# Kernel optimization log

Measured on AMD Instinct MI355X. Metric: run time of the kernel, lower is better.

## Reference

```python
import jax, jax.numpy as jnp
import numpy as np
from math import sqrt

N_HEADS = 16

def _rope(t, freqs):
    # t: [b, n, l, hd]; freqs: [l, hd//2, 2] (real, imag of unit rotations)
    b, n, l, hd = t.shape
    t2 = t.reshape(b, n, l, hd // 2, 2)
    tr, ti = t2[..., 0], t2[..., 1]
    fr, fi = freqs[..., 0], freqs[..., 1]  # broadcast over b, n
    out_r = tr * fr - ti * fi
    out_i = tr * fi + ti * fr
    return jnp.stack([out_r, out_i], axis=-1).reshape(b, n, l, hd)

def setup_inputs() -> dict:
    key = jax.random.key(0)
    ks = jax.random.split(key, 6)
    B, L, D = 2, 2048, 1024
    HD = D // N_HEADS
    x = jax.random.normal(ks[0], (B, L, D), dtype=jnp.float32)
    # proper rotary frequencies: theta_i = 10000^{-2i/hd}, angle = pos * theta
    inv = 1.0 / (10000.0 ** (np.arange(0, HD, 2, dtype=np.float32) / HD))  # [HD//2]
    ang = np.arange(L, dtype=np.float32)[:, None] * inv[None, :]           # [L, HD//2]
    freqs = jnp.asarray(np.stack([np.cos(ang), np.sin(ang)], axis=-1))     # [L, HD//2, 2]
    # additive causal mask
    causal = jnp.tril(jnp.ones((L, L), dtype=bool))
    attention_mask = jnp.where(causal, 0.0, -1e9).astype(jnp.float32)[None, None]
    init = 1.0 / sqrt(D)
    Wq = jax.random.normal(ks[1], (D, D), dtype=jnp.float32) * init
    Wk = jax.random.normal(ks[2], (D, D), dtype=jnp.float32) * init
    Wv = jax.random.normal(ks[3], (D, D), dtype=jnp.float32) * init
    Wo = jax.random.normal(ks[4], (D, D), dtype=jnp.float32) * init
    return {"x": x, "freqs": freqs, "attention_mask": attention_mask,
            "Wq": Wq, "Wk": Wk, "Wv": Wv, "Wo": Wo}

def reference(x, freqs, attention_mask, Wq, Wk, Wv, Wo):
    b, l, d = x.shape
    n = N_HEADS
    hd = d // n
    scale = sqrt(hd)

    def split_heads(t):  # [b, l, d] -> [b, n, l, hd]
        return t.reshape(b, l, n, hd).transpose(0, 2, 1, 3)

    q = split_heads(x @ Wq.T)
    k = split_heads(x @ Wk.T)
    v = split_heads(x @ Wv.T)
    q = _rope(q, freqs)
    k = _rope(k, freqs)
    scores = jnp.einsum('bnqd,bnkd->bnqk', q, k) / scale
    attn = jax.nn.softmax(scores + attention_mask, axis=-1)
    out = jnp.einsum('bnqk,bnkd->bnqd', attn, v)
    out = out.transpose(0, 2, 1, 3).reshape(b, l, d)
    return out @ Wo.T
```

## Files before the change

kernel.cpp:

```cpp
#include <hip/hip_runtime.h>
#include <stdint.h>

#define LSEQ 2048
#define DMODEL 1024
#define NHEADS 16
#define HDIM 64
#define MROWS 4096

typedef __attribute__((ext_vector_type(8))) short short8;
typedef __attribute__((ext_vector_type(4))) float f32x4;
typedef __attribute__((ext_vector_type(16))) float f32x16;

static __device__ __forceinline__ unsigned short f2bf(float f) {
    unsigned u = __builtin_bit_cast(unsigned, f);
    u += 0x7fffu + ((u >> 16) & 1u);
    return (unsigned short)(u >> 16);
}
static __device__ __forceinline__ unsigned packbf2(float a, float b) {
    return (unsigned)f2bf(a) | ((unsigned)f2bf(b) << 16);
}

static __device__ __forceinline__ void gl2lds16(const unsigned short* g, unsigned short* l) {
    __builtin_amdgcn_global_load_lds(
        (const __attribute__((address_space(1))) unsigned int*)g,
        (__attribute__((address_space(3))) unsigned int*)l, 16, 0, 0);
}

__global__ void cast_all(const float* __restrict__ x,  const float* __restrict__ Wq,
                         const float* __restrict__ Wk, const float* __restrict__ Wv,
                         const float* __restrict__ Wo,
                         unsigned short* __restrict__ xb,
                         unsigned short* __restrict__ wqkv,
                         unsigned short* __restrict__ wo) {
    int i = blockIdx.x * blockDim.x + threadIdx.x;
    const float4* src;
    ushort4* dst;
    if (i < 1048576) {
        src = (const float4*)x + i;
        dst = (ushort4*)xb + i;
    } else {
        int t = i - 1048576;
        int w = t >> 18;
        int j = t & 262143;
        const float* s = (w == 0) ? Wq : (w == 1) ? Wk : (w == 2) ? Wv : Wo;
        src = (const float4*)s + j;
        dst = (w == 3) ? ((ushort4*)wo + j) : ((ushort4*)wqkv + (size_t)w * 262144 + j);
    }
    float4 v = *src;
    ushort4 o;
    o.x = f2bf(v.x); o.y = f2bf(v.y); o.z = f2bf(v.z); o.w = f2bf(v.w);
    *dst = o;
}

template <int TM, bool OUT_BF16>
__global__ __launch_bounds__(256) void gemm_nt(const unsigned short* __restrict__ A,
                                               const unsigned short* __restrict__ Bw,
                                               void* __restrict__ C,
                                               int Kdim, int ldc) {
    constexpr int WM = TM / 2;
    __shared__ unsigned short As[TM * 32];
    __shared__ unsigned short Bs[128 * 32];
    int tid = threadIdx.x;
    int lane = tid & 63, wave = tid >> 6;
    int row16 = lane & 15, quad = lane >> 4;
    int wm = wave & 1, wn = wave >> 1;
    int m0 = blockIdx.x * TM;
    int n0 = blockIdx.y * 128;

    int srow = wave * 16 + (lane >> 2);
    int scol = (lane & 3) * 8;
    const unsigned short* Ag = A  + (size_t)(m0 + srow) * Kdim + scol;
    const unsigned short* Bg = Bw + (size_t)(n0 + srow) * Kdim + scol;
    unsigned short* Asw = As + wave * 512;
    unsigned short* Bsw = Bs + wave * 512;

    f32x4 acc[WM / 16][4];
    #pragma unroll
    for (int i = 0; i < WM / 16; ++i)
        #pragma unroll
        for (int j = 0; j < 4; ++j) acc[i][j] = (f32x4){0.f, 0.f, 0.f, 0.f};

    for (int k0 = 0; k0 < Kdim; k0 += 32) {
        #pragma unroll
        for (int i = 0; i < TM / 64; ++i)
            gl2lds16(Ag + (size_t)i * 64 * Kdim + k0, Asw + i * 2048);
        gl2lds16(Bg + k0, Bsw);
        gl2lds16(Bg + (size_t)64 * Kdim + k0, Bsw + 2048);
        __syncthreads();

        short8 af[WM / 16], bf_[4];
        #pragma unroll
        for (int mi = 0; mi < WM / 16; ++mi)
            af[mi] = *(const short8*)(As + (wm * WM + mi * 16 + row16) * 32 + quad * 8);
        #pragma unroll
        for (int ni = 0; ni < 4; ++ni)
            bf_[ni] = *(const short8*)(Bs + (wn * 64 + ni * 16 + row16) * 32 + quad * 8);
        #pragma unroll
        for (int mi = 0; mi < WM / 16; ++mi)
            #pragma unroll
            for (int ni = 0; ni < 4; ++ni)
                acc[mi][ni] = __builtin_amdgcn_mfma_f32_16x16x32_bf16(af[mi], bf_[ni], acc[mi][ni], 0, 0, 0);
        __syncthreads();
    }

    int orow = m0 + wm * WM + quad * 4;
    int ocol = n0 + wn * 64 + row16;
    #pragma unroll
    for (int mi = 0; mi < WM / 16; ++mi)
        #pragma unroll
        for (int ni = 0; ni < 4; ++ni)
            #pragma unroll
            for (int r = 0; r < 4; ++r) {
                size_t idx = (size_t)(orow + mi * 16 + r) * ldc + (ocol + ni * 16);
                if (OUT_BF16) ((unsigned short*)C)[idx] = f2bf(acc[mi][ni][r]);
                else          ((float*)C)[idx]          = acc[mi][ni][r];
            }
}

#define QKV_PHASE(VN, T, DO_STAGE)                                          \
  {                                                                         \
    asm volatile("s_waitcnt vmcnt(" #VN ")" ::: "memory");                  \
    __builtin_amdgcn_s_barrier();                                           \
    __builtin_amdgcn_sched_barrier(0);                                      \
    if (DO_STAGE) {                                                         \
      int t3 = (T) + 3;                                                     \
      int ws = (t3 & 3) * 16384;                                            \
      const unsigned short* asrc = AgL + t3 * 32;                           \
      const unsigned short* bsrc = BgL + t3 * 32;                           \
      gl2lds16(asrc,                        lds + ws + stA);                \
      gl2lds16(asrc + (size_t)128 * DMODEL, lds + ws + stA + 4096);         \
      gl2lds16(bsrc,                        lds + ws + stB);                \
      gl2lds16(bsrc + (size_t)128 * DMODEL, lds + ws + stB + 4096);         \
    }                                                                       \
    {                                                                       \
      int rs = ((T) & 3) * 16384;                                           \
      const unsigned short* Ar = lds + rs + rdA;                            \
      const unsigned short* Br = lds + rs + 8192 + rdB;                     \
      short8 bfr[4];                                                        \
      _Pragma("unroll")                                                     \
      for (int j = 0; j < 4; ++j) bfr[j] = *(const short8*)(Br + j * 512);  \
      _Pragma("unroll")                                                     \
      for (int q = 0; q < 2; ++q) {                                         \
        short8 af[4];                                                       \
        _Pragma("unroll")                                                   \
        for (int i = 0; i < 4; ++i)                                         \
          af[i] = *(const short8*)(Ar + q * 2048 + i * 512);                \
        __builtin_amdgcn_s_setprio(1);                                      \
        _Pragma("unroll")                                                   \
        for (int i = 0; i < 4; ++i)                                         \
          _Pragma("unroll")                                                 \
          for (int j = 0; j < 4; ++j)                                       \
            acc[q * 4 + i][j] = __builtin_amdgcn_mfma_f32_16x16x32_bf16(    \
                af[i], bfr[j], acc[q * 4 + i][j], 0, 0, 0);                 \
        __builtin_amdgcn_s_setprio(0);                                      \
      }                                                                     \
    }                                                                       \
  }

__global__ __launch_bounds__(512, 2) void gemm_qkv(const unsigned short* __restrict__ A,
                                                   const unsigned short* __restrict__ Bw,
                                                   const float* __restrict__ freqs,
                                                   unsigned short* __restrict__ qh,
                                                   unsigned short* __restrict__ kh,
                                                   unsigned short* __restrict__ vt) {
    extern __shared__ unsigned short lds[];

    int tid  = threadIdx.x;
    int lane = tid & 63, wave = tid >> 6;
    int row16 = lane & 15, quad = lane >> 4;
    int wm = wave & 1, wn = wave >> 1;

    int id  = blockIdx.x;
    int gid = (id & 7) * 24 + (id >> 3);
    int bx = gid / 12, by = gid % 12;
    int m0 = bx * 256, n0 = by * 256;

    int off0 = tid * 16;
    int g = off0 ^ (((off0 >> 7) & 3) << 4);
    int srow = g >> 6;
    int scol = (g & 63) >> 1;
    const unsigned short* AgL = A  + (size_t)(m0 + srow) * DMODEL + scol;
    const unsigned short* BgL = Bw + (size_t)(n0 + srow) * DMODEL + scol;

    int stA = wave * 512;
    int stB = 8192 + wave * 512;

    int sw  = ((row16 >> 1) & 3) << 4;
    int rdA = ((((wm * 128 + row16) * 64) + quad * 16) ^ sw) >> 1;
    int rdB = ((((wn *  64 + row16) * 64) + quad * 16) ^ sw) >> 1;

    f32x4 acc[8][4];
    #pragma unroll
    for (int i = 0; i < 8; ++i)
        #pragma unroll
        for (int j = 0; j < 4; ++j) acc[i][j] = (f32x4){0.f, 0.f, 0.f, 0.f};

    #pragma unroll
    for (int p = 0; p < 3; ++p) {
        int ws = p * 16384;
        const unsigned short* asrc = AgL + p * 32;
        const unsigned short* bsrc = BgL + p * 32;
        gl2lds16(asrc,                        lds + ws + stA);
        gl2lds16(asrc + (size_t)128 * DMODEL, lds + ws + stA + 4096);
        gl2lds16(bsrc,                        lds + ws + stB);
        gl2lds16(bsrc + (size_t)128 * DMODEL, lds + ws + stB + 4096);
    }

    for (int t = 0; t < 30; ++t) {
        QKV_PHASE(8, t, (t < 29))
    }
    QKV_PHASE(4, 30, false)
    QKV_PHASE(0, 31, false)

    int region = n0 >> 10;
    int b = m0 >> 11;
    int orow0 = m0 + wm * 128 + quad * 4;
    int ocol0 = n0 + wn * 64 + row16;

    if (region < 2) {
        unsigned short* dst = region ? kh : qh;
        float sgn = (row16 & 1) ? 1.f : -1.f;
        #pragma unroll
        for (int nf = 0; nf < 4; ++nf) {
            int c = ocol0 - region * 1024 + nf * 16;
            int head = c >> 6, d = c & 63, ii = d >> 1;
            unsigned short* hb = dst + ((size_t)(b * NHEADS + head) * LSEQ) * HDIM + d;
            #pragma unroll
            for (int mf = 0; mf < 8; ++mf)
                #pragma unroll
                for (int r = 0; r < 4; ++r) {
                    int l = (orow0 + mf * 16 + r) & 2047;
                    float own = acc[mf][nf][r];
                    float par = __shfl_xor(own, 1);
                    float2 f = *(const float2*)(freqs + ((size_t)l * 32 + ii) * 2);
                    float out = own * f.x + par * (sgn * f.y);
                    hb[(size_t)l * HDIM] = f2bf(out);
                }
        }
    } else {
        #pragma unroll
        for (int nf = 0; nf < 4; ++nf) {
            int c = ocol0 - 2048 + nf * 16;
            int head = c >> 6, d = c & 63;
            size_t vbase = ((size_t)(b * NHEADS + head) * HDIM + d) * LSEQ;
            #pragma unroll
            for (int mf = 0; mf < 8; ++mf) {
                int l0 = (orow0 + mf * 16) & 2047;
                ushort4 o;
                o.x = f2bf(acc[mf][nf][0]);
                o.y = f2bf(acc[mf][nf][1]);
                o.z = f2bf(acc[mf][nf][2]);
                o.w = f2bf(acc[mf][nf][3]);
                *(ushort4*)(vt + vbase + l0) = o;
            }
        }
    }
}

__global__ __launch_bounds__(256, 4) void attn_flash(const unsigned short* __restrict__ qh,
                                                     const unsigned short* __restrict__ kh,
                                                     const unsigned short* __restrict__ vt,
                                                     unsigned short* __restrict__ oh) {
    __shared__ char smem[16896];
    unsigned short* Kbuf = (unsigned short*)smem;
    unsigned short* Vbuf = (unsigned short*)(smem + 8192);
    float* mO = (float*)smem;
    float* mL = (float*)(smem + 16384);
    const float CS = 0.18033688011112042f;
    const float CB = 28.853900817779268f;

    int lane = threadIdx.x & 63;
    int wave = threadIdx.x >> 6;
    int l31 = lane & 31;
    int h   = lane >> 5;
    int kq  = wave >> 1, qq = wave & 1;

    int id  = blockIdx.x;
    int xcd = id & 7;
    int bn  = xcd * 4 + ((id >> 3) & 3);
    int s   = id >> 5;
    int u = s & 7, rnd = s >> 3;
    int qb = (rnd == 0) ? (31 - u) : (rnd == 1) ? (16 + u) : (rnd == 2) ? (15 - u) : u;
    int b = bn >> 4, n = bn & 15;

    const unsigned short* Qb = qh + (size_t)bn * LSEQ * HDIM;
    const unsigned short* Kb = kh + (size_t)bn * LSEQ * HDIM;
    const unsigned short* Vb = vt + (size_t)bn * HDIM * LSEQ;

    int q0 = qb * 64;
    int qabs = q0 + qq * 32 + l31;

    short8 qf[4];
    #pragma unroll
    for (int mf = 0; mf < 4; ++mf)
        qf[mf] = *(const short8*)(Qb + (size_t)(q0 + qq * 32 + l31) * HDIM + mf * 16 + h * 8);

    int sf  = wave >> 1;
    int m0s = (wave & 1) * 2;
    const unsigned short* kg = Kb + (size_t)(sf * 32 + l31) * HDIM + m0s * 16 + h * 8;
    const unsigned short* vg = Vb + (size_t)(sf * 32 + l31) * LSEQ + m0s * 16 + h * 8;
    unsigned short* kds = Kbuf + (sf * 4 + m0s) * 512;
    unsigned short* vds = Vbuf + (sf * 4 + m0s) * 512;

    f32x16 accO[2];
    #pragma unroll
    for (int i = 0; i < 16; ++i) { accO[0][i] = 0.f; accO[1][i] = 0.f; }
    float l_s = 0.f;

    int nk = qb + 1;
    for (int kt = 0; kt < nk; ++kt) {
        const unsigned short* kgk = kg + (size_t)kt * 64 * HDIM;
        const unsigned short* vgk = vg + kt * 64;
        gl2lds16(kgk, kds);       gl2lds16(kgk + 16, kds + 512);
        gl2lds16(vgk, vds);       gl2lds16(vgk + 16, vds + 512);
        __syncthreads();

        bool edge = (kt == nk - 1);
        bool dead = edge && (kq == 1) && (qq == 0);

        if (!dead) {
            f32x16 z;
            #pragma unroll
            for (int i = 0; i < 16; ++i) z[i] = 0.f;
            #pragma unroll
            for (int m = 0; m < 4; ++m) {
                short8 kf = *(const short8*)(Kbuf + (kq * 4 + m) * 512 + lane * 8);
                z = __builtin_amdgcn_mfma_f32_32x32x16_bf16(kf, qf[m], z, 0, 0, 0);
            }

            float p[16];
            bool maskz = edge && (kq == qq);
            #pragma unroll
            for (int r = 0; r < 16; ++r) {
                float e = __builtin_amdgcn_exp2f(z[r] * CS - CB);
                if (maskz) {
                    int kabs = kt * 64 + kq * 32 + (r & 3) + 8 * (r >> 2) + 4 * h;
                    if (kabs > qabs) e = 0.f;
                }
                p[r] = e;
            }
            float ps = 0.f;
            #pragma unroll
            for (int r = 0; r < 16; ++r) ps += p[r];
            l_s += ps;

            uint2 P4[4];
            #pragma unroll
            for (int g = 0; g < 4; ++g) {
                P4[g].x = packbf2(p[4 * g], p[4 * g + 1]);
                P4[g].y = packbf2(p[4 * g + 2], p[4 * g + 3]);
            }
            short8 bfr[2];
            bool hb = (h != 0);
            #pragma unroll
            for (int m = 0; m < 2; ++m) {
                uint2 own = hb ? P4[1 + 2 * m] : P4[2 * m];
                uint2 snd = hb ? P4[2 * m]     : P4[1 + 2 * m];
                uint2 rcv;
                rcv.x = __shfl_xor(snd.x, 32);
                rcv.y = __shfl_xor(snd.y, 32);
                uint4 bb;
                bb.x = hb ? rcv.x : own.x;
                bb.y = hb ? rcv.y : own.y;
                bb.z = hb ? own.x : rcv.x;
                bb.w = hb ? own.y : rcv.y;
                bfr[m] = __builtin_bit_cast(short8, bb);
            }

            #pragma unroll
            for (int dq = 0; dq < 2; ++dq)
                #pragma unroll
                for (int m = 0; m < 2; ++m) {
                    short8 vf = *(const short8*)(Vbuf + (dq * 4 + kq * 2 + m) * 512 + lane * 8);
                    accO[dq] = __builtin_amdgcn_mfma_f32_32x32x16_bf16(vf, bfr[m], accO[dq], 0, 0, 0);
                }
        }
        __syncthreads();
    }

    l_s += __shfl_xor(l_s, 32);

    if (kq == 1) {
        #pragma unroll
        for (int dq = 0; dq < 2; ++dq)
            #pragma unroll
            for (int r = 0; r < 16; ++r)
                mO[(qq * 2 + dq) * 1024 + r * 64 + lane] = accO[dq][r];
        mL[qq * 64 + lane] = l_s;
    }
    __syncthreads();
    if (kq == 0) {
        float inv = 1.0f / (l_s + mL[qq * 64 + lane]);
        #pragma unroll
        for (int dq = 0; dq < 2; ++dq)
            #pragma unroll
            for (int g = 0; g < 4; ++g) {
                float o0 = (accO[dq][4 * g]     + mO[(qq * 2 + dq) * 1024 + (4 * g)     * 64 + lane]) * inv;
                float o1 = (accO[dq][4 * g + 1] + mO[(qq * 2 + dq) * 1024 + (4 * g + 1) * 64 + lane]) * inv;
                float o2 = (accO[dq][4 * g + 2] + mO[(qq * 2 + dq) * 1024 + (4 * g + 2) * 64 + lane]) * inv;
                float o3 = (accO[dq][4 * g + 3] + mO[(qq * 2 + dq) * 1024 + (4 * g + 3) * 64 + lane]) * inv;
                ushort4 o;
                o.x = f2bf(o0); o.y = f2bf(o1); o.z = f2bf(o2); o.w = f2bf(o3);
                int d = dq * 32 + 8 * g + 4 * h;
                *(ushort4*)(oh + (size_t)(b * LSEQ + q0 + qq * 32 + l31) * DMODEL + n * HDIM + d) = o;
            }
    }
}

extern "C" void kernel_launch(void* const* d_in, const int* in_sizes, int n_in,
                              void* d_out, int out_size, void* d_ws, size_t ws_size,
                              hipStream_t stream) {
    const float* x     = (const float*)d_in[0];
    const float* freqs = (const float*)d_in[1];
    const float* Wq = (const float*)d_in[3];
    const float* Wk = (const float*)d_in[4];
    const float* Wv = (const float*)d_in[5];
    const float* Wo = (const float*)d_in[6];

    char* ws = (char*)d_ws;
    unsigned short* xb   = (unsigned short*)ws; ws += (size_t)MROWS * DMODEL * 2;
    unsigned short* wqkv = (unsigned short*)ws; ws += (size_t)3 * DMODEL * DMODEL * 2;
    unsigned short* wo   = (unsigned short*)ws; ws += (size_t)DMODEL * DMODEL * 2;
    unsigned short* qh   = (unsigned short*)ws; ws += (size_t)32 * LSEQ * HDIM * 2;
    unsigned short* kh   = (unsigned short*)ws; ws += (size_t)32 * LSEQ * HDIM * 2;
    unsigned short* vt   = (unsigned short*)ws; ws += (size_t)32 * HDIM * LSEQ * 2;
    unsigned short* oh   = (unsigned short*)ws; ws += (size_t)MROWS * DMODEL * 2;

    static bool attr_set = false;
    if (!attr_set) {
        (void)hipFuncSetAttribute((const void*)gemm_qkv,
                                  hipFuncAttributeMaxDynamicSharedMemorySize, 131072);
        attr_set = true;
    }

    cast_all<<<8192, 256, 0, stream>>>(x, Wq, Wk, Wv, Wo, xb, wqkv, wo);

    gemm_qkv<<<192, 512, 131072, stream>>>(xb, wqkv, freqs, qh, kh, vt);

    attn_flash<<<1024, 256, 0, stream>>>(qh, kh, vt, oh);

    gemm_nt<64, false><<<dim3(MROWS / 64, DMODEL / 128), 256, 0, stream>>>(oh, wo, (float*)d_out, DMODEL, DMODEL);
}
```

Measured before the change: 205.4 us.

## Double-buffer K/V tiles in flash attention with async prefetch two tiles ahead

The attention kernel now keeps two LDS buffers for K and V. It issues global-to-LDS loads two iterations ahead and waits with explicit vmcnt counters, so memory latency overlaps the MFMA and softmax work instead of stalling at a sync every tile. It also raises wave priority around the MFMA blocks and replaces software bf16 rounding with the hardware v_cvt_pk_bf16_f32 instruction. LDS use roughly doubles, which may reduce occupancy at the declared 4 blocks per CU. The hand-written waitcnt logic is fragile if the load count per stage ever changes.

Result: faster. 196.6 us (-4.2%).

```diff
diff --git a/kernel.cpp b/kernel.cpp
--- a/kernel.cpp
+++ b/kernel.cpp
@@ -16,8 +16,10 @@
     u += 0x7fffu + ((u >> 16) & 1u);
     return (unsigned short)(u >> 16);
 }
-static __device__ __forceinline__ unsigned packbf2(float a, float b) {
-    return (unsigned)f2bf(a) | ((unsigned)f2bf(b) << 16);
+static __device__ __forceinline__ unsigned cvt_pk_bf16(float a, float b) {
+    unsigned r;
+    asm("v_cvt_pk_bf16_f32 %0, %1, %2" : "=v"(r) : "v"(a), "v"(b));
+    return r;
 }
 
 static __device__ __forceinline__ void gl2lds16(const unsigned short* g, unsigned short* l) {
@@ -261,9 +263,8 @@
                                                      const unsigned short* __restrict__ kh,
                                                      const unsigned short* __restrict__ vt,
                                                      unsigned short* __restrict__ oh) {
-    __shared__ char smem[16896];
-    unsigned short* Kbuf = (unsigned short*)smem;
-    unsigned short* Vbuf = (unsigned short*)(smem + 8192);
+    __shared__ char smem[33280];
+    unsigned short* ldsb = (unsigned short*)smem;
     float* mO = (float*)smem;
     float* mL = (float*)(smem + 16384);
     const float CS = 0.18033688011112042f;
@@ -299,8 +300,7 @@
     int m0s = (wave & 1) * 2;
     const unsigned short* kg = Kb + (size_t)(sf * 32 + l31) * HDIM + m0s * 16 + h * 8;
     const unsigned short* vg = Vb + (size_t)(sf * 32 + l31) * LSEQ + m0s * 16 + h * 8;
-    unsigned short* kds = Kbuf + (sf * 4 + m0s) * 512;
-    unsigned short* vds = Vbuf + (sf * 4 + m0s) * 512;
+    int soff = (sf * 4 + m0s) * 512;
 
     f32x16 accO[2];
     #pragma unroll
@@ -308,12 +308,29 @@
     float l_s = 0.f;
 
     int nk = qb + 1;
+
+    auto stage = [&](int t) {
+        int sl = (t & 1) * 4096;
+        const unsigned short* kgk = kg + (size_t)t * 64 * HDIM;
+        const unsigned short* vgk = vg + t * 64;
+        gl2lds16(kgk,      ldsb + sl + soff);
+        gl2lds16(kgk + 16, ldsb + sl + soff + 512);
+        gl2lds16(vgk,      ldsb + 8192 + sl + soff);
+        gl2lds16(vgk + 16, ldsb + 8192 + sl + soff + 512);
+    };
+
+    stage(0);
+    stage(1);
+
     for (int kt = 0; kt < nk; ++kt) {
-        const unsigned short* kgk = kg + (size_t)kt * 64 * HDIM;
-        const unsigned short* vgk = vg + kt * 64;
-        gl2lds16(kgk, kds);       gl2lds16(kgk + 16, kds + 512);
-        gl2lds16(vgk, vds);       gl2lds16(vgk + 16, vds + 512);
-        __syncthreads();
+        if (kt < nk - 1) asm volatile("s_waitcnt vmcnt(4)" ::: "memory");
+        else             asm volatile("s_waitcnt vmcnt(0)" ::: "memory");
+        __builtin_amdgcn_s_barrier();
+        __builtin_amdgcn_sched_barrier(0);
+
+        int cb = (kt & 1) * 4096;
+        const unsigned short* Kc = ldsb + cb;
+        const unsigned short* Vc = ldsb + 8192 + cb;
 
         bool edge = (kt == nk - 1);
         bool dead = edge && (kq == 1) && (qq == 0);
@@ -322,11 +339,13 @@
             f32x16 z;
             #pragma unroll
             for (int i = 0; i < 16; ++i) z[i] = 0.f;
+            __builtin_amdgcn_s_setprio(1);
             #pragma unroll
             for (int m = 0; m < 4; ++m) {
-                short8 kf = *(const short8*)(Kbuf + (kq * 4 + m) * 512 + lane * 8);
+                short8 kf = *(const short8*)(Kc + (kq * 4 + m) * 512 + lane * 8);
                 z = __builtin_amdgcn_mfma_f32_32x32x16_bf16(kf, qf[m], z, 0, 0, 0);
             }
+            __builtin_amdgcn_s_setprio(0);
 
             float p[16];
             bool maskz = edge && (kq == qq);
@@ -347,8 +366,8 @@
             uint2 P4[4];
             #pragma unroll
             for (int g = 0; g < 4; ++g) {
-                P4[g].x = packbf2(p[4 * g], p[4 * g + 1]);
-                P4[g].y = packbf2(p[4 * g + 2], p[4 * g + 3]);
+                P4[g].x = cvt_pk_bf16(p[4 * g],     p[4 * g + 1]);
+                P4[g].y = cvt_pk_bf16(p[4 * g + 2], p[4 * g + 3]);
             }
             short8 bfr[2];
             bool hb = (h != 0);
@@ -367,15 +386,20 @@
                 bfr[m] = __builtin_bit_cast(short8, bb);
             }
 
+            __builtin_amdgcn_s_setprio(1);
             #pragma unroll
             for (int dq = 0; dq < 2; ++dq)
                 #pragma unroll
                 for (int m = 0; m < 2; ++m) {
-                    short8 vf = *(const short8*)(Vbuf + (dq * 4 + kq * 2 + m) * 512 + lane * 8);
+                    short8 vf = *(const short8*)(Vc + (dq * 4 + kq * 2 + m) * 512 + lane * 8);
                     accO[dq] = __builtin_amdgcn_mfma_f32_32x32x16_bf16(vf, bfr[m], accO[dq], 0, 0, 0);
                 }
+            __builtin_amdgcn_s_setprio(0);
         }
-        __syncthreads();
+
+        __builtin_amdgcn_sched_barrier(0);
+        __builtin_amdgcn_s_barrier();
+        if (kt + 2 < nk) stage(kt + 2);
     }
 
     l_s += __shfl_xor(l_s, 32);
```
